# Kernel tuning notes

Measured on AMD Instinct MI355X. Metric: run time of the kernel, lower is better.

## Reference

```python
import jax, jax.numpy as jnp
import numpy as np

# ---- maxflat pyramid filters (pfilters('maxflat')) ----
def _maxflat_filters():
    sqrt2 = np.sqrt(2.0)
    M1 = M2 = 1.0 / sqrt2
    k1 = 1.0 - sqrt2
    k2 = k3 = M1
    h_half = np.array([0.25 * k2 * k3, 0.5 * k2, 1.0 + 0.5 * k2 * k3]) * M1
    h = np.concatenate([h_half, h_half[:-1][::-1]]) * sqrt2          # len 5
    g_half = np.array([-0.125 * k1 * k2 * k3,
                       0.25 * k1 * k2,
                       -0.5 * k1 - 0.5 * k3 - 0.375 * k1 * k2 * k3,
                       1.0 + 0.5 * k1 * k2]) * M2
    g = np.concatenate([g_half, g_half[:-1][::-1]]) * sqrt2          # len 7
    return h.astype(np.float32), g.astype(np.float32)

# highpass from g, as in wfb2dec: h1 = -g * (-1)**(arange(1,L+1)-c)
def _wfb_filters():
    h, g = _maxflat_filters()
    len_h1 = len(g)                      # 7 (odd)
    c = int(np.floor((len_h1 + 1.0) / 2.0))   # 4
    h1 = (-g * (-1.0) ** (np.arange(1, len_h1 + 1) - c)).astype(np.float32)
    ext_h0 = int(np.floor(len(h) / 2.0))      # 2
    ext_h1 = len_h1 - c + 1                   # 4
    return h, h1, ext_h0, ext_h1

# periodic row filtering along last axis (torch rowfiltering: periodic pad +
# cross-correlation, which F.conv2d / lax conv both compute without flip)
def rowfilt(x, f, ext1):
    L = f.shape[0]
    ext2 = L - ext1 - 1
    W = x.shape[-1]
    xe = jnp.concatenate([x[..., -ext1:], x, x[..., :ext2]], axis=-1)
    y = f[0] * xe[..., 0:W]
    for k in range(1, L):                 # tiny fixed tap loop, fuses fine
        y = y + f[k] * xe[..., k:k + W]
    return y

def colfilt(x, f, ext1):
    return jnp.swapaxes(rowfilt(jnp.swapaxes(x, -1, -2), f, ext1), -1, -2)


def setup_inputs() -> dict:
    key = jax.random.key(0)
    x = jax.random.normal(key, (8, 3, 1024, 1024), dtype=jnp.float32)
    return {"x": x}


def reference(x):
    # Pycontourlet.batch_multi_channel_pdfbdec with pfilt='maxflat',
    # nlevs=[0] -> wfb2dec path: one level of separable wavelet FB with
    # periodic extension; returns [xLL, [xLH, xHL, xHH]] (stacked here).
    h_np, h1_np, e0, e1 = _wfb_filters()
    h = jnp.asarray(h_np)
    h1 = jnp.asarray(h1_np)

    x_L = rowfilt(x, h, e0)[..., ::2]          # [B,C,H,W/2]
    x_H = rowfilt(x, h1, e1)[..., ::2]

    x_LL = colfilt(x_L, h, e0)[..., ::2, :]    # [B,C,H/2,W/2]
    x_LH = colfilt(x_L, h1, e1)[..., ::2, :]
    x_HL = colfilt(x_H, h, e0)[..., ::2, :]
    x_HH = colfilt(x_H, h1, e1)[..., ::2, :]

    return jnp.stack([x_LL, x_LH, x_HL, x_HH])  # [4,B,C,H/2,W/2]
```

## Files before the change

### kernel.cpp

```cpp
#include <hip/hip_runtime.h>


constexpr int H = 1024, W = 1024;
constexpr int NIMG = 24;
constexpr int HOUT = 512, WOUT = 512;
constexpr int TO = 32;
constexpr int RIN = 69;
constexpr int PAD = 34;

__global__ __launch_bounds__(256)
void wfb_kernel(const float* __restrict__ x, float* __restrict__ out) {
    __shared__ float s_L[RIN][PAD];
    __shared__ float s_H[RIN][PAD];

    const float h0c[5] = {0.125f, 0.35355339059327373f, 1.25f,
                          0.35355339059327373f, 0.125f};
    const float h1c[7] = {0.025888347648318447f,  0.07322330470336313f,
                          -0.06878156646177083f, -0.8535533905932737f,
                          -0.06878156646177083f,  0.07322330470336313f,
                          0.025888347648318447f};

    const int tid = threadIdx.x;
    const int img = blockIdx.z;
    const int r0 = blockIdx.y * TO;
    const int c0 = blockIdx.x * TO;
    const float* __restrict__ xin = x + (size_t)img * H * W;
    const int rbase = 2 * r0 - 4;
    const int cbase = 2 * c0 - 4;

    for (int m = tid; m < RIN * TO; m += 256) {
        int r = m >> 5;
        int j = m & 31;
        int gr = (rbase + r) & (H - 1);
        const float* __restrict__ rowp = xin + (size_t)gr * W;
        int b = cbase + 2 * j;
        float v0 = rowp[(b + 0) & (W - 1)];
        float v1 = rowp[(b + 1) & (W - 1)];
        float v2 = rowp[(b + 2) & (W - 1)];
        float v3 = rowp[(b + 3) & (W - 1)];
        float v4 = rowp[(b + 4) & (W - 1)];
        float v5 = rowp[(b + 5) & (W - 1)];
        float v6 = rowp[(b + 6) & (W - 1)];
        s_L[r][j] = h0c[0]*v2 + h0c[1]*v3 + h0c[2]*v4 + h0c[3]*v5 + h0c[4]*v6;
        s_H[r][j] = h1c[0]*v0 + h1c[1]*v1 + h1c[2]*v2 + h1c[3]*v3
                  + h1c[4]*v4 + h1c[5]*v5 + h1c[6]*v6;
    }
    __syncthreads();

    constexpr size_t SB = (size_t)NIMG * HOUT * WOUT;
    float* __restrict__ o = out + (size_t)img * HOUT * WOUT;
    for (int m = tid; m < TO * (TO / 2); m += 256) {
        int i  = m >> 4;
        int jj = (m & 15) * 2;
        float LLx = 0.f, LLy = 0.f, HLx = 0.f, HLy = 0.f;
        float LHx = 0.f, LHy = 0.f, HHx = 0.f, HHy = 0.f;
        #pragma unroll
        for (int k = 0; k < 5; ++k) {
            float a0 = s_L[2*i + 2 + k][jj], a1 = s_L[2*i + 2 + k][jj + 1];
            float b0 = s_H[2*i + 2 + k][jj], b1 = s_H[2*i + 2 + k][jj + 1];
            LLx += h0c[k] * a0;  LLy += h0c[k] * a1;
            HLx += h0c[k] * b0;  HLy += h0c[k] * b1;
        }
        #pragma unroll
        for (int k = 0; k < 7; ++k) {
            float a0 = s_L[2*i + k][jj], a1 = s_L[2*i + k][jj + 1];
            float b0 = s_H[2*i + k][jj], b1 = s_H[2*i + k][jj + 1];
            LHx += h1c[k] * a0;  LHy += h1c[k] * a1;
            HHx += h1c[k] * b0;  HHy += h1c[k] * b1;
        }
        size_t off = (size_t)(r0 + i) * WOUT + (c0 + jj);
        *(float2*)(o + 0 * SB + off) = make_float2(LLx, LLy);
        *(float2*)(o + 1 * SB + off) = make_float2(LHx, LHy);
        *(float2*)(o + 2 * SB + off) = make_float2(HLx, HLy);
        *(float2*)(o + 3 * SB + off) = make_float2(HHx, HHy);
    }
}

extern "C" void kernel_launch(void* const* d_in, const int* in_sizes, int n_in,
                              void* d_out, int out_size, void* d_ws, size_t ws_size,
                              hipStream_t stream) {
    const float* x = (const float*)d_in[0];
    float* out = (float*)d_out;
    dim3 grid(WOUT / TO, HOUT / TO, NIMG);
    wfb_kernel<<<grid, dim3(256), 0, stream>>>(x, out);
}
```

Baseline: 207.2 us.

## Vectorize row-filter loads and column-filter outputs with float4 register blocking

The horizontal pass now has each thread load 24 contiguous input floats as six float4 reads and compute 8 lowpass and 8 highpass outputs, replacing seven scalar loads per output. The vertical pass has each thread produce 4 columns with float4 shared-memory reads and float4 global stores. The shared row pitch grows to 36 so float4 accesses stay 16-byte aligned. Only 276 threads' worth of work fills the first phase, so most threads of the 256-thread block sit idle for part of it, and bank conflicts on the wider LDS accesses may shift.

```diff
diff --git a/kernel.cpp b/kernel.cpp
--- a/kernel.cpp
+++ b/kernel.cpp
@@ -6,7 +6,7 @@
 constexpr int HOUT = 512, WOUT = 512;
 constexpr int TO = 32;
 constexpr int RIN = 69;
-constexpr int PAD = 34;
+constexpr int PAD = 36;
 
 __global__ __launch_bounds__(256)
 void wfb_kernel(const float* __restrict__ x, float* __restrict__ out) {
@@ -28,51 +28,63 @@
     const int rbase = 2 * r0 - 4;
     const int cbase = 2 * c0 - 4;
 
-    for (int m = tid; m < RIN * TO; m += 256) {
-        int r = m >> 5;
-        int j = m & 31;
+    for (int m = tid; m < RIN * 4; m += 256) {
+        int r = m >> 2;
+        int g = m & 3;
         int gr = (rbase + r) & (H - 1);
         const float* __restrict__ rowp = xin + (size_t)gr * W;
-        int b = cbase + 2 * j;
-        float v0 = rowp[(b + 0) & (W - 1)];
-        float v1 = rowp[(b + 1) & (W - 1)];
-        float v2 = rowp[(b + 2) & (W - 1)];
-        float v3 = rowp[(b + 3) & (W - 1)];
-        float v4 = rowp[(b + 4) & (W - 1)];
-        float v5 = rowp[(b + 5) & (W - 1)];
-        float v6 = rowp[(b + 6) & (W - 1)];
-        s_L[r][j] = h0c[0]*v2 + h0c[1]*v3 + h0c[2]*v4 + h0c[3]*v5 + h0c[4]*v6;
-        s_H[r][j] = h1c[0]*v0 + h1c[1]*v1 + h1c[2]*v2 + h1c[3]*v3
-                  + h1c[4]*v4 + h1c[5]*v5 + h1c[6]*v6;
+        int b0 = cbase + 16 * g;
+        float v[24];
+        #pragma unroll
+        for (int t = 0; t < 6; ++t) {
+            int gc = (b0 + 4 * t) & (W - 1);
+            float4 f = *(const float4*)(rowp + gc);
+            v[4*t + 0] = f.x; v[4*t + 1] = f.y;
+            v[4*t + 2] = f.z; v[4*t + 3] = f.w;
+        }
+        float Lo[8], Ho[8];
+        #pragma unroll
+        for (int u = 0; u < 8; ++u) {
+            const float* p = v + 2 * u;
+            Lo[u] = h0c[0]*p[2] + h0c[1]*p[3] + h0c[2]*p[4]
+                  + h0c[3]*p[5] + h0c[4]*p[6];
+            Ho[u] = h1c[0]*p[0] + h1c[1]*p[1] + h1c[2]*p[2] + h1c[3]*p[3]
+                  + h1c[4]*p[4] + h1c[5]*p[5] + h1c[6]*p[6];
+        }
+        int j0 = 8 * g;
+        *(float4*)&s_L[r][j0]     = make_float4(Lo[0], Lo[1], Lo[2], Lo[3]);
+        *(float4*)&s_L[r][j0 + 4] = make_float4(Lo[4], Lo[5], Lo[6], Lo[7]);
+        *(float4*)&s_H[r][j0]     = make_float4(Ho[0], Ho[1], Ho[2], Ho[3]);
+        *(float4*)&s_H[r][j0 + 4] = make_float4(Ho[4], Ho[5], Ho[6], Ho[7]);
     }
     __syncthreads();
 
     constexpr size_t SB = (size_t)NIMG * HOUT * WOUT;
     float* __restrict__ o = out + (size_t)img * HOUT * WOUT;
-    for (int m = tid; m < TO * (TO / 2); m += 256) {
-        int i  = m >> 4;
-        int jj = (m & 15) * 2;
-        float LLx = 0.f, LLy = 0.f, HLx = 0.f, HLy = 0.f;
-        float LHx = 0.f, LHy = 0.f, HHx = 0.f, HHy = 0.f;
+    {
+        int i  = tid >> 3;
+        int jj = (tid & 7) * 4;
+        float LLx=0,LLy=0,LLz=0,LLw=0, HLx=0,HLy=0,HLz=0,HLw=0;
+        float LHx=0,LHy=0,LHz=0,LHw=0, HHx=0,HHy=0,HHz=0,HHw=0;
         #pragma unroll
         for (int k = 0; k < 5; ++k) {
-            float a0 = s_L[2*i + 2 + k][jj], a1 = s_L[2*i + 2 + k][jj + 1];
-            float b0 = s_H[2*i + 2 + k][jj], b1 = s_H[2*i + 2 + k][jj + 1];
-            LLx += h0c[k] * a0;  LLy += h0c[k] * a1;
-            HLx += h0c[k] * b0;  HLy += h0c[k] * b1;
+            float4 a = *(const float4*)&s_L[2*i + 2 + k][jj];
+            float4 b = *(const float4*)&s_H[2*i + 2 + k][jj];
+            LLx += h0c[k]*a.x; LLy += h0c[k]*a.y; LLz += h0c[k]*a.z; LLw += h0c[k]*a.w;
+            HLx += h0c[k]*b.x; HLy += h0c[k]*b.y; HLz += h0c[k]*b.z; HLw += h0c[k]*b.w;
         }
         #pragma unroll
         for (int k = 0; k < 7; ++k) {
-            float a0 = s_L[2*i + k][jj], a1 = s_L[2*i + k][jj + 1];
-            float b0 = s_H[2*i + k][jj], b1 = s_H[2*i + k][jj + 1];
-            LHx += h1c[k] * a0;  LHy += h1c[k] * a1;
-            HHx += h1c[k] * b0;  HHy += h1c[k] * b1;
+            float4 a = *(const float4*)&s_L[2*i + k][jj];
+            float4 b = *(const float4*)&s_H[2*i + k][jj];
+            LHx += h1c[k]*a.x; LHy += h1c[k]*a.y; LHz += h1c[k]*a.z; LHw += h1c[k]*a.w;
+            HHx += h1c[k]*b.x; HHy += h1c[k]*b.y; HHz += h1c[k]*b.z; HHw += h1c[k]*b.w;
         }
         size_t off = (size_t)(r0 + i) * WOUT + (c0 + jj);
-        *(float2*)(o + 0 * SB + off) = make_float2(LLx, LLy);
-        *(float2*)(o + 1 * SB + off) = make_float2(LHx, LHy);
-        *(float2*)(o + 2 * SB + off) = make_float2(HLx, HLy);
-        *(float2*)(o + 3 * SB + off) = make_float2(HHx, HHy);
+        *(float4*)(o + 0 * SB + off) = make_float4(LLx, LLy, LLz, LLw);
+        *(float4*)(o + 1 * SB + off) = make_float4(LHx, LHy, LHz, LHw);
+        *(float4*)(o + 2 * SB + off) = make_float4(HLx, HLy, HLz, HLw);
+        *(float4*)(o + 3 * SB + off) = make_float4(HHx, HHy, HHz, HHw);
     }
 }
 
```

Measured after the change: 182.3 us. 12.0% less time.
